# Kernel optimization log

Measured on AMD Instinct MI355X. Metric: run time of the kernel, lower is better.

## Reference

```python
import jax, jax.numpy as jnp
import numpy as np

BN_EPS = 1e-5


def conv1x1(x, w, b):
    # x: [B,C,H,W], w: [O,C], b: [O]
    return jnp.einsum('oc,bchw->bohw', w, x) + b[None, :, None, None]


def setup_inputs() -> dict:
    key = jax.random.key(0)
    ks = jax.random.split(key, 8)
    B, C, H, W = 4, 256, 64, 64
    Ci = C // 2  # inter_channels
    std = 0.01
    return {
        'x': jax.random.normal(ks[0], (B, C, H, W), dtype=jnp.float32),
        'w_g': jax.random.normal(ks[1], (Ci, C), dtype=jnp.float32) * std,
        'b_g': jnp.zeros((Ci,), jnp.float32),
        'w_theta': jax.random.normal(ks[2], (Ci, C), dtype=jnp.float32) * std,
        'b_theta': jnp.zeros((Ci,), jnp.float32),
        'w_phi': jax.random.normal(ks[3], (Ci, C), dtype=jnp.float32) * std,
        'b_phi': jnp.zeros((Ci,), jnp.float32),
        'w_out': jax.random.normal(ks[4], (C, Ci), dtype=jnp.float32) * std,
        'b_out': jnp.zeros((C,), jnp.float32),
        'bn_gamma': jax.random.normal(ks[5], (C,), dtype=jnp.float32),
        'bn_beta': jnp.zeros((C,), jnp.float32),
    }


def reference(x, w_g, b_g, w_theta, b_theta, w_phi, b_phi, w_out, b_out, bn_gamma, bn_beta):
    B, C, H, W = x.shape
    Ci = w_g.shape[0]
    N = H * W
    # 1x1 conv projections -> flatten spatial to tokens
    g_x = conv1x1(x, w_g, b_g).reshape(B, Ci, N)          # [B,Ci,N]
    theta_x = conv1x1(x, w_theta, b_theta).reshape(B, Ci, N)
    phi_x = conv1x1(x, w_phi, b_phi).reshape(B, Ci, N)
    # dense non-causal attention over N=HW tokens (no scaling)
    f = jnp.einsum('bcn,bcm->bnm', theta_x, phi_x)        # [B,N,N]
    f_div_C = jax.nn.softmax(f, axis=-1)
    y = jnp.einsum('bnm,bcm->bcn', f_div_C, g_x)          # [B,Ci,N]
    y = y.reshape(B, Ci, H, W)
    # output 1x1 conv + BatchNorm2d (training mode: batch statistics)
    W_y = conv1x1(y, w_out, b_out)                        # [B,C,H,W]
    mean = W_y.mean(axis=(0, 2, 3))
    var = W_y.var(axis=(0, 2, 3))
    W_y = (W_y - mean[None, :, None, None]) * jax.lax.rsqrt(var + BN_EPS)[None, :, None, None]
    W_y = W_y * bn_gamma[None, :, None, None] + bn_beta[None, :, None, None]
    return W_y + x
```

## Files before the change

### kernel.cpp

```cpp
#include <hip/hip_runtime.h>

#define N_TOK 4096
#define C_IN 256
#define CI_ 128

typedef unsigned short u16;
typedef unsigned int   u32;
typedef __attribute__((ext_vector_type(8))) short bf16x8;
typedef __attribute__((ext_vector_type(4))) float f32x4;

__device__ __forceinline__ float lo16f(u32 u){ union{u32 i; float f;} c; c.i = u << 16; return c.f; }
__device__ __forceinline__ float hi16f(u32 u){ union{u32 i; float f;} c; c.i = u & 0xffff0000u; return c.f; }
__device__ __forceinline__ void bf8f(const uint4 u, float* f){
    f[0]=lo16f(u.x); f[1]=hi16f(u.x); f[2]=lo16f(u.y); f[3]=hi16f(u.y);
    f[4]=lo16f(u.z); f[5]=hi16f(u.z); f[6]=lo16f(u.w); f[7]=hi16f(u.w);
}
__device__ __forceinline__ float bf1f(u16 v){ union{u32 i; float f;} c; c.i = ((u32)v)<<16; return c.f; }
__device__ __forceinline__ u16 f2bf(float f){
    union{float f; u32 i;} c; c.f = f;
    u32 i = c.i;
    u32 r = (i + 0x7fffu + ((i >> 16) & 1u)) >> 16;
    return (u16)r;
}
__device__ __forceinline__ u32 packbf(float a, float b){
    return (u32)f2bf(a) | ((u32)f2bf(b) << 16);
}

__device__ __forceinline__ void load8(const void* base, size_t idx, int flag, float* f){
    if (flag) {
        const float* p = (const float*)base + idx;
        *(float4*)&f[0] = *(const float4*)p;
        *(float4*)&f[4] = *(const float4*)(p + 4);
    } else {
        uint4 u = *(const uint4*)((const u16*)base + idx);
        bf8f(u, f);
    }
}
__device__ __forceinline__ void load4(const void* base, size_t idx, int flag, float* f){
    if (flag) {
        float4 v = *(const float4*)((const float*)base + idx);
        f[0]=v.x; f[1]=v.y; f[2]=v.z; f[3]=v.w;
    } else {
        uint2 u = *(const uint2*)((const u16*)base + idx);
        f[0]=lo16f(u.x); f[1]=hi16f(u.x); f[2]=lo16f(u.y); f[3]=hi16f(u.y);
    }
}

__device__ __forceinline__ void dma16(const u16* g, char* l){
    __builtin_amdgcn_global_load_lds(
        (const __attribute__((address_space(1))) u32*)g,
        (__attribute__((address_space(3))) u32*)l, 16, 0, 0);
}

__global__ __launch_bounds__(256) void convert_params_kernel(
    const void* wg, const void* wt, const void* wp, const void* wo,
    const void* bg, const void* bt, const void* bp, const void* bo,
    const void* gm, const void* bt2,
    int* __restrict__ flagp, float* __restrict__ canon, u16* __restrict__ canon_bf,
    float* __restrict__ stats)
{
    __shared__ int sflag;
    const int tid = threadIdx.x;
    if (tid < 64) {
        int cnt = 0;
        const u16* wgp = (const u16*)wg;
        for (int i = tid; i < 256; i += 64) {
            u16 v = wgp[2 * i];
            if (((v >> 7) & 0xFF) >= 128) cnt++;
        }
        #pragma unroll
        for (int off = 32; off; off >>= 1) cnt += __shfl_down(cnt, off);
        if (tid == 0) sflag = (cnt >= 8) ? 1 : 0;
    }
    __syncthreads();
    const int f = sflag;
    if (blockIdx.x == 0 && tid == 0) *flagp = f;

    int idx = blockIdx.x * 256 + tid;
    if (idx >= 132224) {
        int j = idx - 132224;
        if (j < 4096) stats[j] = 0.f;
        return;
    }
    const void* src; int loc;
    if      (idx < 32768)  { src = wg;  loc = idx; }
    else if (idx < 65536)  { src = wt;  loc = idx - 32768; }
    else if (idx < 98304)  { src = wp;  loc = idx - 65536; }
    else if (idx < 131072) { src = wo;  loc = idx - 98304; }
    else if (idx < 131200) { src = bg;  loc = idx - 131072; }
    else if (idx < 131328) { src = bt;  loc = idx - 131200; }
    else if (idx < 131456) { src = bp;  loc = idx - 131328; }
    else if (idx < 131712) { src = bo;  loc = idx - 131456; }
    else if (idx < 131968) { src = gm;  loc = idx - 131712; }
    else                   { src = bt2; loc = idx - 131968; }
    float v = f ? ((const float*)src)[loc] : bf1f(((const u16*)src)[loc]);
    canon[idx] = v;
    if (idx < 131072) canon_bf[idx] = f2bf(v);
}

__global__ __launch_bounds__(256) void xpose_kernel(
    const void* __restrict__ x, const int* __restrict__ flagp, u16* __restrict__ xbfT)
{
    __shared__ u16 t[64][72];
    const int flag = *flagp;
    const int b = blockIdx.z, k0 = blockIdx.y * 64, n0 = blockIdx.x * 64;
    const int tid = threadIdx.x;
    const size_t xb = (size_t)b * C_IN * N_TOK;
    {
        int kk = tid >> 4, n4 = (tid & 15) * 4;
        #pragma unroll
        for (int i = 0; i < 4; ++i) {
            float f[4];
            load4(x, xb + (size_t)(k0 + kk + i * 16) * N_TOK + n0 + n4, flag, f);
            #pragma unroll
            for (int j = 0; j < 4; ++j) t[n4 + j][kk + i * 16] = f2bf(f[j]);
        }
    }
    __syncthreads();
    {
        int kq = tid & 3, n = tid >> 2;
        u16* dst = &xbfT[((size_t)b * N_TOK + n0 + n) * C_IN + k0 + kq * 16];
        *(uint4*)(dst + 0) = *(const uint4*)&t[n][kq * 16];
        *(uint4*)(dst + 8) = *(const uint4*)&t[n][kq * 16 + 8];
    }
}

__global__ __launch_bounds__(512) void proj_kernel(
    const u16* __restrict__ xbfT, const float* __restrict__ canon,
    const u16* __restrict__ wbf,
    u16* __restrict__ gbuf, u16* __restrict__ tbufT, u16* __restrict__ pbufT)
{
    __shared__ __align__(16) u16 plds[64 * 400];
    const int b  = blockIdx.y;
    const int n0 = blockIdx.x * 64;
    const int tid = threadIdx.x;
    const int w    = tid >> 6;
    const int lane = tid & 63;
    const int col  = lane & 15;
    const int quad = lane >> 4;
    const int rw   = w * 48;
    const size_t bN = (size_t)b * N_TOK;

    f32x4 acc[3][4];
    #pragma unroll
    for (int i = 0; i < 3; ++i)
        #pragma unroll
        for (int j = 0; j < 4; ++j) acc[i][j] = (f32x4){0.f,0.f,0.f,0.f};

    #pragma unroll
    for (int kc = 0; kc < 8; ++kc) {
        bf16x8 bfr[4];
        #pragma unroll
        for (int nf = 0; nf < 4; ++nf)
            bfr[nf] = *(const bf16x8*)&xbfT[(bN + n0 + nf * 16 + col) * C_IN + kc * 32 + quad * 8];
        #pragma unroll
        for (int rs = 0; rs < 3; ++rs) {
            bf16x8 afr = *(const bf16x8*)&wbf[(size_t)(rw + rs * 16 + col) * 256 + kc * 32 + quad * 8];
            #pragma unroll
            for (int nf = 0; nf < 4; ++nf)
                acc[rs][nf] = __builtin_amdgcn_mfma_f32_16x16x32_bf16(afr, bfr[nf], acc[rs][nf], 0, 0, 0);
        }
    }

    #pragma unroll
    for (int rs = 0; rs < 3; ++rs) {
        int r0 = rw + rs * 16 + quad * 4;
        float b0 = canon[131072 + r0 + 0];
        float b1 = canon[131072 + r0 + 1];
        float b2 = canon[131072 + r0 + 2];
        float b3 = canon[131072 + r0 + 3];
        #pragma unroll
        for (int nf = 0; nf < 4; ++nf) {
            int n = nf * 16 + col;
            uint2 pv;
            pv.x = packbf(acc[rs][nf][0] + b0, acc[rs][nf][1] + b1);
            pv.y = packbf(acc[rs][nf][2] + b2, acc[rs][nf][3] + b3);
            *(uint2*)&plds[n * 400 + r0] = pv;
        }
    }
    __syncthreads();

    {
        int r = tid & 127, nq = tid >> 7;
        u16 tmp[16];
        #pragma unroll
        for (int j = 0; j < 16; ++j) tmp[j] = plds[(nq * 16 + j) * 400 + r];
        u16* dst = &gbuf[((size_t)b * CI_ + r) * N_TOK + n0 + nq * 16];
        *(uint4*)(dst + 0) = *(uint4*)&tmp[0];
        *(uint4*)(dst + 8) = *(uint4*)&tmp[8];
    }
    {
        int n = tid & 63, part = tid >> 6;
        const u16* src = (part < 4) ? &plds[n * 400 + 128 + part * 32]
                                    : &plds[n * 400 + 256 + (part - 4) * 32];
        u16* dst = (part < 4) ? &tbufT[(bN + n0 + n) * CI_ + part * 32]
                              : &pbufT[(bN + n0 + n) * CI_ + (part - 4) * 32];
        #pragma unroll
        for (int v = 0; v < 4; ++v) *(uint4*)(dst + v * 8) = *(const uint4*)(src + v * 8);
    }
}

#define PB2   131072
#define MST2  147456
#define LST2  147712
#define SMEM2 147968

__global__ __launch_bounds__(512) void attn_kernel(
    const u16* __restrict__ tbufT, const u16* __restrict__ pbufT,
    const u16* __restrict__ gbuf,
    const u16* __restrict__ wbf, const float* __restrict__ canon,
    u16* __restrict__ wyb, float* __restrict__ stats)
{
    __shared__ __align__(16) char smem[SMEM2];
    const int b   = blockIdx.y;
    const int q0  = blockIdx.x * 64;
    const int tid = threadIdx.x;
    const int w    = tid >> 6;
    const int lane = tid & 63;
    const int col  = lane & 15;
    const int quad = lane >> 4;
    const int wq   = w & 3;
    const int ms   = w >> 2;
    const int qw   = wq * 16;
    const size_t bN = (size_t)b * N_TOK;
    const size_t bC = (size_t)b * CI_;

    bf16x8 thf[4];
    {
        const u16* tb = tbufT + (bN + q0 + qw + col) * CI_;
        #pragma unroll
        for (int kc = 0; kc < 4; ++kc)
            thf[kc] = *(const bf16x8*)(tb + kc * 32 + quad * 8);
    }

    const u16* sb[8];
    int ldso[8];
    int sstep;
    if (w < 4) {
        int r = lane >> 4, cp = lane & 15;
        sstep = 128 * CI_;
        #pragma unroll
        for (int j = 0; j < 8; ++j) {
            int seg = w * 8 + j, p = seg >> 4, m0 = (seg & 15) * 4;
            int m = m0 + r, h = cp ^ (m & 15);
            sb[j] = pbufT + (bN + p * 64 + m) * CI_ + h * 8;
            ldso[j] = p * 16384 + m0 * 256;
        }
    } else {
        int r = lane >> 3, cp = lane & 7;
        sstep = 128;
        #pragma unroll
        for (int j = 0; j < 8; ++j) {
            int seg = (w - 4) * 8 + j, p = seg >> 4, c0 = (seg & 15) * 8;
            int c = c0 + r, h = cp ^ (c & 7);
            sb[j] = gbuf + (bC + c) * N_TOK + p * 64 + h * 8;
            ldso[j] = 65536 + p * 16384 + c0 * 128;
        }
    }

    f32x4 yacc[8];
    #pragma unroll
    for (int i = 0; i < 8; ++i) yacc[i] = (f32x4){0.f, 0.f, 0.f, 0.f};
    float m_st = -3.0e38f, l_st = 0.f;

    #pragma unroll
    for (int j = 0; j < 8; ++j) dma16(sb[j], smem + ldso[j]);

    for (int s = 0; s < 32; ++s) {
        const int bb = (s & 1) << 15;
        __asm volatile("s_waitcnt lgkmcnt(0)" ::: "memory");
        __asm volatile("s_barrier" ::: "memory");
        if (s < 31) {
            const int nb = ((s + 1) & 1) << 15;
            const size_t so = (size_t)(s + 1) * sstep;
            #pragma unroll
            for (int j = 0; j < 8; ++j) dma16(sb[j] + so, smem + nb + ldso[j]);
            __asm volatile("s_waitcnt vmcnt(8)" ::: "memory");
        } else {
            __asm volatile("s_waitcnt vmcnt(0)" ::: "memory");
        }
        __asm volatile("s_barrier" ::: "memory");

        f32x4 sacc[4];
        #pragma unroll
        for (int i = 0; i < 4; ++i) sacc[i] = (f32x4){0.f, 0.f, 0.f, 0.f};
        #pragma unroll
        for (int kc = 0; kc < 4; ++kc) {
            #pragma unroll
            for (int msub = 0; msub < 4; ++msub) {
                int m = msub * 16 + col;
                int h = kc * 4 + quad;
                bf16x8 af = *(const bf16x8*)(smem + bb + ms * 16384 + m * 256 + ((h ^ (m & 15)) << 4));
                sacc[msub] = __builtin_amdgcn_mfma_f32_16x16x32_bf16(af, thf[kc], sacc[msub], 0, 0, 0);
            }
        }

        float tmax = sacc[0][0];
        #pragma unroll
        for (int i = 0; i < 4; ++i)
            #pragma unroll
            for (int r = 0; r < 4; ++r) tmax = fmaxf(tmax, sacc[i][r]);
        tmax = fmaxf(tmax, __shfl_xor(tmax, 16));
        tmax = fmaxf(tmax, __shfl_xor(tmax, 32));
        float m_new = fmaxf(m_st, tmax);
        float p16[16], ps = 0.f;
        #pragma unroll
        for (int i = 0; i < 4; ++i)
            #pragma unroll
            for (int r = 0; r < 4; ++r) {
                float pv = __expf(sacc[i][r] - m_new);
                p16[i * 4 + r] = pv;
                ps += pv;
            }
        ps += __shfl_xor(ps, 16);
        ps += __shfl_xor(ps, 32);
        float alpha = __expf(m_st - m_new);
        l_st = l_st * alpha + ps;
        m_st = m_new;
        #pragma unroll
        for (int i = 0; i < 8; ++i) {
            yacc[i][0] *= alpha; yacc[i][1] *= alpha;
            yacc[i][2] *= alpha; yacc[i][3] *= alpha;
        }

        {
            char* pb = smem + PB2 + w * 2048 + col * 128;
            #pragma unroll
            for (int msub = 0; msub < 4; ++msub) {
                #pragma unroll
                for (int pr = 0; pr < 2; ++pr) {
                    u32 d = packbf(p16[msub * 4 + pr * 2], p16[msub * 4 + pr * 2 + 1]);
                    int h = msub * 2 + (quad >> 1);
                    *(u32*)(pb + ((h ^ (col & 7)) << 4) + (quad & 1) * 8 + pr * 4) = d;
                }
            }
        }
        __asm volatile("s_waitcnt lgkmcnt(0)" ::: "memory");

        bf16x8 pf[2];
        #pragma unroll
        for (int km = 0; km < 2; ++km) {
            int h = km * 4 + quad;
            pf[km] = *(const bf16x8*)(smem + PB2 + w * 2048 + col * 128 + ((h ^ (col & 7)) << 4));
        }
        #pragma unroll
        for (int csub = 0; csub < 8; ++csub) {
            #pragma unroll
            for (int km = 0; km < 2; ++km) {
                int c = csub * 16 + col;
                int h = km * 4 + quad;
                bf16x8 gf = *(const bf16x8*)(smem + 65536 + bb + ms * 16384 + c * 128 + ((h ^ (c & 7)) << 4));
                yacc[csub] = __builtin_amdgcn_mfma_f32_16x16x32_bf16(gf, pf[km], yacc[csub], 0, 0, 0);
            }
        }
    }

    __syncthreads();
    if (ms == 1) {
        char* mb = smem + wq * 8192 + col * 512;
        #pragma unroll
        for (int csub = 0; csub < 8; ++csub)
            *(f32x4*)(mb + (((csub * 4 + quad) ^ col) << 4)) = yacc[csub];
        if (quad == 0) {
            *(float*)(smem + MST2 + (wq * 16 + col) * 4) = m_st;
            *(float*)(smem + LST2 + (wq * 16 + col) * 4) = l_st;
        }
    }
    __syncthreads();
    if (ms == 0) {
        float m1 = *(const float*)(smem + MST2 + (wq * 16 + col) * 4);
        float l1 = *(const float*)(smem + LST2 + (wq * 16 + col) * 4);
        float M  = fmaxf(m_st, m1);
        float a0 = __expf(m_st - M), a1 = __expf(m1 - M);
        float li = 1.f / (l_st * a0 + l1 * a1);
        float s0 = a0 * li, s1 = a1 * li;
        const char* mb = smem + wq * 8192 + col * 512;
        const int q = qw + col;
        #pragma unroll
        for (int csub = 0; csub < 8; ++csub) {
            f32x4 y1 = *(const f32x4*)(mb + (((csub * 4 + quad) ^ col) << 4));
            uint2 pv;
            pv.x = packbf(yacc[csub][0] * s0 + y1[0] * s1, yacc[csub][1] * s0 + y1[1] * s1);
            pv.y = packbf(yacc[csub][2] * s0 + y1[2] * s1, yacc[csub][3] * s0 + y1[3] * s1);
            int chunk = csub * 2 + (quad >> 1);
            *(uint2*)(smem + 32768 + q * 256 + ((chunk ^ (q & 15)) << 4) + (quad & 1) * 8) = pv;
        }
    }
    __syncthreads();

    const u16* wo = wbf + 98304;
    f32x4 oacc[2][4];
    #pragma unroll
    for (int i = 0; i < 2; ++i)
        #pragma unroll
        for (int j = 0; j < 4; ++j) oacc[i][j] = (f32x4){0.f,0.f,0.f,0.f};
    #pragma unroll
    for (int kc = 0; kc < 4; ++kc) {
        bf16x8 bqf[4];
        #pragma unroll
        for (int qf = 0; qf < 4; ++qf) {
            int q = qf * 16 + col;
            int h = kc * 4 + quad;
            bqf[qf] = *(const bf16x8*)(smem + 32768 + q * 256 + ((h ^ (q & 15)) << 4));
        }
        #pragma unroll
        for (int os = 0; os < 2; ++os) {
            bf16x8 afr = *(const bf16x8*)&wo[(size_t)(w * 32 + os * 16 + col) * CI_ + kc * 32 + quad * 8];
            #pragma unroll
            for (int qf = 0; qf < 4; ++qf)
                oacc[os][qf] = __builtin_amdgcn_mfma_f32_16x16x32_bf16(afr, bqf[qf], oacc[os][qf], 0, 0, 0);
        }
    }
    const int bucket = (blockIdx.x + blockIdx.y) & 7;
    float* sbk = stats + bucket * 512;
    #pragma unroll
    for (int os = 0; os < 2; ++os) {
        int ob = w * 32 + os * 16 + quad * 4;
        #pragma unroll
        for (int i = 0; i < 4; ++i) {
            float bb2 = canon[131456 + ob + i];
            float s1 = 0.f, s2 = 0.f;
            u16* dst = &wyb[((size_t)b * C_IN + ob + i) * N_TOK + q0 + col];
            #pragma unroll
            for (int qf = 0; qf < 4; ++qf) {
                float v = oacc[os][qf][i] + bb2;
                dst[qf * 16] = f2bf(v);
                s1 += v;
                s2 += v * v;
            }
            #pragma unroll
            for (int off = 8; off; off >>= 1) {
                s1 += __shfl_xor(s1, off);
                s2 += __shfl_xor(s2, off);
            }
            if (col == 0) {
                atomicAdd(&sbk[ob + i], s1);
                atomicAdd(&sbk[256 + ob + i], s2);
            }
        }
    }
}

__global__ __launch_bounds__(256) void bnorm_kernel(
    const u16* __restrict__ wyb, const void* __restrict__ x,
    const float* __restrict__ stats,
    const float* __restrict__ canon, const int* __restrict__ flagp,
    void* __restrict__ outv)
{
    const int flag = *flagp;
    size_t base = ((size_t)blockIdx.x * 256 + threadIdx.x) * 8;
    int o = (int)((base >> 12) & 255);
    float sum1 = 0.f, sum2 = 0.f;
    #pragma unroll
    for (int k = 0; k < 8; ++k) {
        sum1 += stats[k * 512 + o];
        sum2 += stats[k * 512 + 256 + o];
    }
    float mean = sum1 * (1.f / 16384.f);
    float var  = sum2 * (1.f / 16384.f) - mean * mean;
    float r = rsqrtf(var + 1e-5f);
    float gm = canon[131712 + o], bt = canon[131968 + o];
    uint4 wu = *(const uint4*)&wyb[base];
    float wv[8]; bf8f(wu, wv);
    float xf[8]; load8(x, base, flag, xf);
    float ov[8];
    #pragma unroll
    for (int i = 0; i < 8; ++i)
        ov[i] = (wv[i] - mean) * r * gm + bt + xf[i];
    if (flag) {
        float* op = (float*)outv + base;
        *(float4*)op       = *(float4*)&ov[0];
        *(float4*)(op + 4) = *(float4*)&ov[4];
    } else {
        uint4 res;
        res.x = packbf(ov[0], ov[1]);
        res.y = packbf(ov[2], ov[3]);
        res.z = packbf(ov[4], ov[5]);
        res.w = packbf(ov[6], ov[7]);
        *(uint4*)((u16*)outv + base) = res;
    }
}

extern "C" void kernel_launch(void* const* d_in, const int* in_sizes, int n_in,
                              void* d_out, int out_size, void* d_ws, size_t ws_size,
                              hipStream_t stream)
{
    const void* x   = d_in[0];
    const void* w_g = d_in[1];
    const void* b_g = d_in[2];
    const void* w_t = d_in[3];
    const void* b_t = d_in[4];
    const void* w_p = d_in[5];
    const void* b_p = d_in[6];
    const void* w_o = d_in[7];
    const void* b_o = d_in[8];
    const void* gm  = d_in[9];
    const void* bt  = d_in[10];

    char* base = (char*)d_ws;
    float* canon    = (float*)base;
    u16*   canon_bf = (u16*)(base + 528896);
    int*   flagp    = (int*)(base + 791040);
    float* stats    = (float*)(base + 791296);
    u16*   gbuf     = (u16*)(base + 1048576);
    u16*   tbufT    = (u16*)(base + 5242880);
    u16*   pbufT    = (u16*)(base + 9437184);
    u16*   wyb      = (u16*)(base + 13631488);
    u16*   xbfT     = (u16*)(base + 22020096);

    convert_params_kernel<<<533, 256, 0, stream>>>(w_g, w_t, w_p, w_o, b_g, b_t, b_p, b_o,
                                                   gm, bt, flagp, canon, canon_bf, stats);
    xpose_kernel<<<dim3(64, 4, 4), 256, 0, stream>>>(x, flagp, xbfT);
    proj_kernel<<<dim3(64, 4), 512, 0, stream>>>(xbfT, canon, canon_bf, gbuf, tbufT, pbufT);
    attn_kernel<<<dim3(64, 4), 512, 0, stream>>>(tbufT, pbufT, gbuf, canon_bf, canon, wyb, stats);
    bnorm_kernel<<<2048, 256, 0, stream>>>(wyb, x, stats, canon, flagp, d_out);
}
```

Measured before the change: 188.0 us.

## Halve attention block to 32 queries and 4 waves to double grid size

The attention kernel now processes 32 query rows per block with 256 threads instead of 64 rows with 512 threads. This doubles the grid from 256 to 512 blocks and cuts shared memory from about 148KB to about 70KB, so more blocks can be resident per CU and all CUs of the device get work. Key/value tiles shrink to 32 tokens with a new swizzle, the loop runs 64 steps instead of 32, and the BN stats buckets grow to 16 to spread atomics. In exchange, each key/value tile is loaded twice as often per query, and each step carries more barrier overhead relative to its MFMA work.

```diff
diff --git a/kernel.cpp b/kernel.cpp
--- a/kernel.cpp
+++ b/kernel.cpp
@@ -79,7 +79,7 @@
     int idx = blockIdx.x * 256 + tid;
     if (idx >= 132224) {
         int j = idx - 132224;
-        if (j < 4096) stats[j] = 0.f;
+        if (j < 8192) stats[j] = 0.f;
         return;
     }
     const void* src; int loc;
@@ -200,27 +200,29 @@
     }
 }
 
-#define PB2   131072
-#define MST2  147456
-#define LST2  147712
-#define SMEM2 147968
-
-__global__ __launch_bounds__(512) void attn_kernel(
+#define PH3   0
+#define G3    32768
+#define PB3   65536
+#define MST3  69632
+#define LST3  69760
+#define SMEM3 69888
+
+__global__ __launch_bounds__(256) void attn_kernel(
     const u16* __restrict__ tbufT, const u16* __restrict__ pbufT,
     const u16* __restrict__ gbuf,
     const u16* __restrict__ wbf, const float* __restrict__ canon,
     u16* __restrict__ wyb, float* __restrict__ stats)
 {
-    __shared__ __align__(16) char smem[SMEM2];
+    __shared__ __align__(16) char smem[SMEM3];
     const int b   = blockIdx.y;
-    const int q0  = blockIdx.x * 64;
+    const int q0  = blockIdx.x * 32;
     const int tid = threadIdx.x;
     const int w    = tid >> 6;
     const int lane = tid & 63;
     const int col  = lane & 15;
     const int quad = lane >> 4;
-    const int wq   = w & 3;
-    const int ms   = w >> 2;
+    const int wq   = w & 1;
+    const int ms   = w >> 1;
     const int qw   = wq * 16;
     const size_t bN = (size_t)b * N_TOK;
     const size_t bC = (size_t)b * CI_;
@@ -236,25 +238,27 @@
     const u16* sb[8];
     int ldso[8];
     int sstep;
-    if (w < 4) {
+    if (w < 2) {
         int r = lane >> 4, cp = lane & 15;
-        sstep = 128 * CI_;
+        sstep = 64 * CI_;
         #pragma unroll
         for (int j = 0; j < 8; ++j) {
-            int seg = w * 8 + j, p = seg >> 4, m0 = (seg & 15) * 4;
-            int m = m0 + r, h = cp ^ (m & 15);
-            sb[j] = pbufT + (bN + p * 64 + m) * CI_ + h * 8;
-            ldso[j] = p * 16384 + m0 * 256;
+            int seg = w * 8 + j;
+            int par = seg >> 3, m0 = (seg & 7) * 4;
+            int m = m0 + r;
+            sb[j] = pbufT + (bN + par * 32 + m) * CI_ + (cp ^ (m & 15)) * 8;
+            ldso[j] = PH3 + par * 8192 + m0 * 256;
         }
     } else {
-        int r = lane >> 3, cp = lane & 7;
-        sstep = 128;
+        int r = lane >> 2, cp = lane & 3;
+        sstep = 64;
         #pragma unroll
         for (int j = 0; j < 8; ++j) {
-            int seg = (w - 4) * 8 + j, p = seg >> 4, c0 = (seg & 15) * 8;
-            int c = c0 + r, h = cp ^ (c & 7);
-            sb[j] = gbuf + (bC + c) * N_TOK + p * 64 + h * 8;
-            ldso[j] = 65536 + p * 16384 + c0 * 128;
+            int seg = (w - 2) * 8 + j;
+            int par = seg >> 3, c0 = (seg & 7) * 16;
+            int c = c0 + r;
+            sb[j] = gbuf + (bC + c) * N_TOK + par * 32 + (cp ^ ((c >> 1) & 3)) * 8;
+            ldso[j] = G3 + par * 8192 + c0 * 64;
         }
     }
 
@@ -266,12 +270,12 @@
     #pragma unroll
     for (int j = 0; j < 8; ++j) dma16(sb[j], smem + ldso[j]);
 
-    for (int s = 0; s < 32; ++s) {
-        const int bb = (s & 1) << 15;
+    for (int s = 0; s < 64; ++s) {
+        const int bb = (s & 1) << 14;
         __asm volatile("s_waitcnt lgkmcnt(0)" ::: "memory");
         __asm volatile("s_barrier" ::: "memory");
-        if (s < 31) {
-            const int nb = ((s + 1) & 1) << 15;
+        if (s < 63) {
+            const int nb = ((s + 1) & 1) << 14;
             const size_t so = (size_t)(s + 1) * sstep;
             #pragma unroll
             for (int j = 0; j < 8; ++j) dma16(sb[j] + so, smem + nb + ldso[j]);
@@ -281,31 +285,31 @@
         }
         __asm volatile("s_barrier" ::: "memory");
 
-        f32x4 sacc[4];
-        #pragma unroll
-        for (int i = 0; i < 4; ++i) sacc[i] = (f32x4){0.f, 0.f, 0.f, 0.f};
+        f32x4 sacc[2];
+        sacc[0] = (f32x4){0.f, 0.f, 0.f, 0.f};
+        sacc[1] = (f32x4){0.f, 0.f, 0.f, 0.f};
         #pragma unroll
         for (int kc = 0; kc < 4; ++kc) {
             #pragma unroll
-            for (int msub = 0; msub < 4; ++msub) {
+            for (int msub = 0; msub < 2; ++msub) {
                 int m = msub * 16 + col;
                 int h = kc * 4 + quad;
-                bf16x8 af = *(const bf16x8*)(smem + bb + ms * 16384 + m * 256 + ((h ^ (m & 15)) << 4));
+                bf16x8 af = *(const bf16x8*)(smem + PH3 + bb + ms * 8192 + m * 256 + ((h ^ (m & 15)) << 4));
                 sacc[msub] = __builtin_amdgcn_mfma_f32_16x16x32_bf16(af, thf[kc], sacc[msub], 0, 0, 0);
             }
         }
 
         float tmax = sacc[0][0];
         #pragma unroll
-        for (int i = 0; i < 4; ++i)
+        for (int i = 0; i < 2; ++i)
             #pragma unroll
             for (int r = 0; r < 4; ++r) tmax = fmaxf(tmax, sacc[i][r]);
         tmax = fmaxf(tmax, __shfl_xor(tmax, 16));
         tmax = fmaxf(tmax, __shfl_xor(tmax, 32));
         float m_new = fmaxf(m_st, tmax);
-        float p16[16], ps = 0.f;
-        #pragma unroll
-        for (int i = 0; i < 4; ++i)
+        float p16[8], ps = 0.f;
+        #pragma unroll
+        for (int i = 0; i < 2; ++i)
             #pragma unroll
             for (int r = 0; r < 4; ++r) {
                 float pv = __expf(sacc[i][r] - m_new);
@@ -324,34 +328,26 @@
         }
 
         {
-            char* pb = smem + PB2 + w * 2048 + col * 128;
-            #pragma unroll
-            for (int msub = 0; msub < 4; ++msub) {
+            char* pb = smem + PB3 + w * 1024 + col * 64;
+            const int swz = (col >> 1) & 3;
+            #pragma unroll
+            for (int msub = 0; msub < 2; ++msub) {
                 #pragma unroll
                 for (int pr = 0; pr < 2; ++pr) {
                     u32 d = packbf(p16[msub * 4 + pr * 2], p16[msub * 4 + pr * 2 + 1]);
-                    int h = msub * 2 + (quad >> 1);
-                    *(u32*)(pb + ((h ^ (col & 7)) << 4) + (quad & 1) * 8 + pr * 4) = d;
+                    int hl = msub * 2 + (quad >> 1);
+                    *(u32*)(pb + ((hl ^ swz) << 4) + (quad & 1) * 8 + pr * 4) = d;
                 }
             }
         }
         __asm volatile("s_waitcnt lgkmcnt(0)" ::: "memory");
 
-        bf16x8 pf[2];
-        #pragma unroll
-        for (int km = 0; km < 2; ++km) {
-            int h = km * 4 + quad;
-            pf[km] = *(const bf16x8*)(smem + PB2 + w * 2048 + col * 128 + ((h ^ (col & 7)) << 4));
-        }
+        bf16x8 pf = *(const bf16x8*)(smem + PB3 + w * 1024 + col * 64 + ((quad ^ ((col >> 1) & 3)) << 4));
         #pragma unroll
         for (int csub = 0; csub < 8; ++csub) {
-            #pragma unroll
-            for (int km = 0; km < 2; ++km) {
-                int c = csub * 16 + col;
-                int h = km * 4 + quad;
-                bf16x8 gf = *(const bf16x8*)(smem + 65536 + bb + ms * 16384 + c * 128 + ((h ^ (c & 7)) << 4));
-                yacc[csub] = __builtin_amdgcn_mfma_f32_16x16x32_bf16(gf, pf[km], yacc[csub], 0, 0, 0);
-            }
+            int c = csub * 16 + col;
+            bf16x8 gf = *(const bf16x8*)(smem + G3 + bb + ms * 8192 + c * 64 + ((quad ^ ((c >> 1) & 3)) << 4));
+            yacc[csub] = __builtin_amdgcn_mfma_f32_16x16x32_bf16(gf, pf, yacc[csub], 0, 0, 0);
         }
     }
 
@@ -362,14 +358,14 @@
         for (int csub = 0; csub < 8; ++csub)
             *(f32x4*)(mb + (((csub * 4 + quad) ^ col) << 4)) = yacc[csub];
         if (quad == 0) {
-            *(float*)(smem + MST2 + (wq * 16 + col) * 4) = m_st;
-            *(float*)(smem + LST2 + (wq * 16 + col) * 4) = l_st;
+            *(float*)(smem + MST3 + (qw + col) * 4) = m_st;
+            *(float*)(smem + LST3 + (qw + col) * 4) = l_st;
         }
     }
     __syncthreads();
     if (ms == 0) {
-        float m1 = *(const float*)(smem + MST2 + (wq * 16 + col) * 4);
-        float l1 = *(const float*)(smem + LST2 + (wq * 16 + col) * 4);
+        float m1 = *(const float*)(smem + MST3 + (qw + col) * 4);
+        float l1 = *(const float*)(smem + LST3 + (qw + col) * 4);
         float M  = fmaxf(m_st, m1);
         float a0 = __expf(m_st - M), a1 = __expf(m1 - M);
         float li = 1.f / (l_st * a0 + l1 * a1);
@@ -389,40 +385,41 @@
     __syncthreads();
 
     const u16* wo = wbf + 98304;
-    f32x4 oacc[2][4];
-    #pragma unroll
-    for (int i = 0; i < 2; ++i)
-        #pragma unroll
-        for (int j = 0; j < 4; ++j) oacc[i][j] = (f32x4){0.f,0.f,0.f,0.f};
+    f32x4 oacc[4][2];
+    #pragma unroll
+    for (int i = 0; i < 4; ++i) {
+        oacc[i][0] = (f32x4){0.f,0.f,0.f,0.f};
+        oacc[i][1] = (f32x4){0.f,0.f,0.f,0.f};
+    }
     #pragma unroll
     for (int kc = 0; kc < 4; ++kc) {
-        bf16x8 bqf[4];
-        #pragma unroll
-        for (int qf = 0; qf < 4; ++qf) {
+        bf16x8 bqf[2];
+        #pragma unroll
+        for (int qf = 0; qf < 2; ++qf) {
             int q = qf * 16 + col;
             int h = kc * 4 + quad;
             bqf[qf] = *(const bf16x8*)(smem + 32768 + q * 256 + ((h ^ (q & 15)) << 4));
         }
         #pragma unroll
-        for (int os = 0; os < 2; ++os) {
-            bf16x8 afr = *(const bf16x8*)&wo[(size_t)(w * 32 + os * 16 + col) * CI_ + kc * 32 + quad * 8];
-            #pragma unroll
-            for (int qf = 0; qf < 4; ++qf)
+        for (int os = 0; os < 4; ++os) {
+            bf16x8 afr = *(const bf16x8*)&wo[(size_t)(w * 64 + os * 16 + col) * CI_ + kc * 32 + quad * 8];
+            #pragma unroll
+            for (int qf = 0; qf < 2; ++qf)
                 oacc[os][qf] = __builtin_amdgcn_mfma_f32_16x16x32_bf16(afr, bqf[qf], oacc[os][qf], 0, 0, 0);
         }
     }
-    const int bucket = (blockIdx.x + blockIdx.y) & 7;
+    const int bucket = (blockIdx.x + blockIdx.y) & 15;
     float* sbk = stats + bucket * 512;
     #pragma unroll
-    for (int os = 0; os < 2; ++os) {
-        int ob = w * 32 + os * 16 + quad * 4;
+    for (int os = 0; os < 4; ++os) {
+        int ob = w * 64 + os * 16 + quad * 4;
         #pragma unroll
         for (int i = 0; i < 4; ++i) {
             float bb2 = canon[131456 + ob + i];
             float s1 = 0.f, s2 = 0.f;
             u16* dst = &wyb[((size_t)b * C_IN + ob + i) * N_TOK + q0 + col];
             #pragma unroll
-            for (int qf = 0; qf < 4; ++qf) {
+            for (int qf = 0; qf < 2; ++qf) {
                 float v = oacc[os][qf][i] + bb2;
                 dst[qf * 16] = f2bf(v);
                 s1 += v;
@@ -452,7 +449,7 @@
     int o = (int)((base >> 12) & 255);
     float sum1 = 0.f, sum2 = 0.f;
     #pragma unroll
-    for (int k = 0; k < 8; ++k) {
+    for (int k = 0; k < 16; ++k) {
         sum1 += stats[k * 512 + o];
         sum2 += stats[k * 512 + 256 + o];
     }
@@ -508,10 +505,10 @@
     u16*   wyb      = (u16*)(base + 13631488);
     u16*   xbfT     = (u16*)(base + 22020096);
 
-    convert_params_kernel<<<533, 256, 0, stream>>>(w_g, w_t, w_p, w_o, b_g, b_t, b_p, b_o,
+    convert_params_kernel<<<549, 256, 0, stream>>>(w_g, w_t, w_p, w_o, b_g, b_t, b_p, b_o,
                                                    gm, bt, flagp, canon, canon_bf, stats);
     xpose_kernel<<<dim3(64, 4, 4), 256, 0, stream>>>(x, flagp, xbfT);
     proj_kernel<<<dim3(64, 4), 512, 0, stream>>>(xbfT, canon, canon_bf, gbuf, tbufT, pbufT);
-    attn_kernel<<<dim3(64, 4), 512, 0, stream>>>(tbufT, pbufT, gbuf, canon_bf, canon, wyb, stats);
+    attn_kernel<<<dim3(128, 4), 256, 0, stream>>>(tbufT, pbufT, gbuf, canon_bf, canon, wyb, stats);
     bnorm_kernel<<<2048, 256, 0, stream>>>(wyb, x, stats, canon, flagp, d_out);
 }
```

New measurement: 218.9 us. 16.5% more time.
